# Kernel optimization log

Hardware: AMD Instinct MI355X
Metric: run time of the kernel (lower is better)

Reference implementation:

```python
import jax, jax.numpy as jnp
import numpy as np
from jax import lax

L, B, D = 2048, 16, 1024

def setup_inputs() -> dict:
    key = jax.random.key(0)
    k1, k2, k3 = jax.random.split(key, 3)
    prev_layer = jax.random.normal(k1, (L, B, D), dtype=jnp.float32)
    hidden = jax.random.normal(k2, (B, D), dtype=jnp.float32)
    W = jax.random.normal(k3, (3 * D, D), dtype=jnp.float32) * (1.0 / np.sqrt(D))
    b = jnp.zeros((3 * D,), dtype=jnp.float32)
    return {"prev_layer": prev_layer, "hidden": hidden, "W": W, "b": b}

def reference(prev_layer, hidden, W, b):
    # prev_layer: [L, B, D], hidden: [B, D], W: [3D, D], b: [3D]
    d = hidden.shape[-1]
    # nn.Linear: y = x @ W.T + b  (dropout p=0 -> identity)
    preact = jnp.einsum('lbi,oi->lbo', prev_layer, W) + b  # [L, B, 3D]
    x_t = preact[..., :d]                                   # candidate
    gates = jax.nn.sigmoid(preact[..., d:])                 # [L, B, 2D]
    z = gates[..., :d]
    h_gate = gates[..., d:]

    def step(h, zx):
        zt, xt = zx
        s = (1.0 - zt) * h + zt * xt
        return s, s

    hidden_final, ss = lax.scan(step, hidden, (z, x_t))     # ss: [L, B, D]
    out = (1.0 - h_gate) * ss + h_gate * prev_layer         # highway (input_size==output_size)
    return out, hidden_final
```

## Files before the change

### kernel.cpp

```cpp
#include <hip/hip_runtime.h>
#include <cstdint>

#define L_DIM 2048
#define B_DIM 16
#define D_DIM 1024
#define M_DIM (L_DIM*B_DIM)
#define N_DIM (3*D_DIM)
#define K_DIM D_DIM
#define NCH   (B_DIM*D_DIM)
#define SEG   64
#define SEGLEN (L_DIM/SEG)
#define CG    (NCH/8)

#define BK 64
#define NKT (K_DIM/BK)
#define BUF 65536

typedef __bf16 bf16x8 __attribute__((ext_vector_type(8)));
typedef float f32x4 __attribute__((ext_vector_type(4)));

__device__ inline float bf2f(ushort u){ return __uint_as_float(((unsigned)u)<<16); }
__device__ inline ushort f2bf(float f){
  unsigned u = __float_as_uint(f);
  u += 0x7fffu + ((u>>16)&1u);
  return (ushort)(u>>16);
}

__global__ __launch_bounds__(256) void cvt8(const float* __restrict__ in,
                                            ushort* __restrict__ out, int n8){
  int t = blockIdx.x*256 + threadIdx.x;
  if (t >= n8) return;
  const float4* p = (const float4*)(in + (size_t)t*8);
  float4 a = p[0], b = p[1];
  ushort r[8] = {f2bf(a.x),f2bf(a.y),f2bf(a.z),f2bf(a.w),
                 f2bf(b.x),f2bf(b.y),f2bf(b.z),f2bf(b.w)};
  *(uint4*)(out + (size_t)t*8) = *(const uint4*)r;
}

#define GLOAD(gp, lp) __builtin_amdgcn_global_load_lds( \
    (const __attribute__((address_space(1))) void*)(gp), \
    (__attribute__((address_space(3))) void*)(lp), 16, 0, 0)

__global__ __launch_bounds__(512, 2) void gemm_sru(
    const ushort* __restrict__ gA,
    const ushort* __restrict__ gB,
    const float* __restrict__ bias,
    ushort* __restrict__ xbuf, ushort* __restrict__ zbuf, ushort* __restrict__ hbuf)
{
  __shared__ ulong2 lds_[2*BUF/16];
  char* ldsb = (char*)lds_;

  const int tid  = threadIdx.x;
  const int lane = tid & 63, w = tid >> 6;
  const int wr = (w>>2)*64;
  const int wc = (w&3)*32;

  const int bid = blockIdx.x;
  const int swz = (bid & 7)*192 + (bid >> 3);
  const int bm = (swz / (N_DIM/256))*256, bn = (swz % (N_DIM/256))*256;

  const int l15 = lane & 15, l4 = lane >> 4, l7 = lane & 7;
  const int s0 = ((l4)     ^ l7) * 16;
  const int s1 = ((4 + l4) ^ l7) * 16;
  const char* pA0 = ldsb + (wr + l15)*128 + s0;
  const char* pA1 = ldsb + (wr + l15)*128 + s1;
  const char* pB0 = ldsb + 32768 + (wc + l15)*128 + s0;
  const char* pB1 = ldsb + 32768 + (wc + l15)*128 + s1;

  const int gks = (tid & 7) ^ ((tid >> 3) & 7);
  const size_t gArow = (size_t)(bm + (tid>>3))*K_DIM + gks*8;
  const size_t gBrow = (size_t)(bn + (tid>>3))*K_DIM + gks*8;

  f32x4 acc[4][8];
  #pragma unroll
  for (int i=0;i<4;i++)
    #pragma unroll
    for (int j=0;j<8;j++) acc[i][j] = (f32x4){0.f,0.f,0.f,0.f};

#define STAGE_A(h, tt) do{ \
    const ushort* g = gA + gArow + (size_t)(h)*128*K_DIM + (tt)*BK; \
    char* d = ldsb + ((tt)&1)*BUF + (h)*16384 + tid*16; \
    GLOAD(g, d); GLOAD(g + (size_t)64*K_DIM, d + 8192); \
  }while(0)
#define STAGE_B(h, tt) do{ \
    const ushort* g = gB + gBrow + (size_t)(h)*128*K_DIM + (tt)*BK; \
    char* d = ldsb + ((tt)&1)*BUF + 32768 + (h)*16384 + tid*16; \
    GLOAD(g, d); GLOAD(g + (size_t)64*K_DIM, d + 8192); \
  }while(0)

#define RD_A(dst, QA, bo) { _Pragma("unroll") \
    for (int fr=0; fr<4; ++fr){ \
      dst[fr][0] = *(const bf16x8*)(pA0 + (bo) + (QA)*16384 + fr*2048); \
      dst[fr][1] = *(const bf16x8*)(pA1 + (bo) + (QA)*16384 + fr*2048); } }
#define RD_B(QB, bo) { _Pragma("unroll") \
    for (int fc=0; fc<2; ++fc){ \
      b[fc][0] = *(const bf16x8*)(pB0 + (bo) + (QB)*16384 + fc*2048); \
      b[fc][1] = *(const bf16x8*)(pB1 + (bo) + (QB)*16384 + fc*2048); } }
#define MFMA_Q(qi, asrc) { \
    __builtin_amdgcn_s_setprio(1); \
    _Pragma("unroll") \
    for (int fr=0; fr<4; ++fr) \
      _Pragma("unroll") \
      for (int fc=0; fc<2; ++fc){ \
        acc[qi][fr*2+fc] = __builtin_amdgcn_mfma_f32_16x16x32_bf16(asrc[fr][0], b[fc][0], acc[qi][fr*2+fc], 0,0,0); \
        acc[qi][fr*2+fc] = __builtin_amdgcn_mfma_f32_16x16x32_bf16(asrc[fr][1], b[fc][1], acc[qi][fr*2+fc], 0,0,0); } \
    __builtin_amdgcn_s_setprio(0); }
#define BAR() asm volatile("" ::: "memory"); __builtin_amdgcn_s_barrier(); asm volatile("" ::: "memory")
#define VM(n) asm volatile("s_waitcnt vmcnt(" #n ")" ::: "memory")

  bf16x8 a0[4][2], a1[4][2], b[2][2];

  STAGE_A(0,0); STAGE_B(0,0); STAGE_A(1,0); STAGE_B(1,0);
  VM(4); BAR();

  for (int t = 0; t < NKT-1; ++t) {
    const int bo = (t&1)*BUF;
    RD_A(a0, 0, bo); RD_B(0, bo);
    STAGE_A(0, t+1);
    VM(4); BAR();
    MFMA_Q(0, a0); BAR();
    RD_A(a1, 1, bo);
    STAGE_B(0, t+1);
    VM(4); BAR();
    MFMA_Q(2, a1); BAR();
    RD_B(1, bo);
    STAGE_A(1, t+1);
    VM(6); BAR();
    MFMA_Q(3, a1); BAR();
    STAGE_B(1, t+1);
    VM(4); BAR();
    MFMA_Q(1, a0); BAR();
  }
  {
    const int bo = ((NKT-1)&1)*BUF;
    RD_A(a0, 0, bo); RD_B(0, bo);
    VM(2); BAR();
    MFMA_Q(0, a0); BAR();
    RD_A(a1, 1, bo);
    VM(0); BAR();
    MFMA_Q(2, a1); BAR();
    RD_B(1, bo);
    BAR();
    MFMA_Q(3, a1); BAR();
    MFMA_Q(1, a0); BAR();
  }

  const int region = bn >> 10;
  ushort* dst = region==0 ? xbuf : (region==1 ? zbuf : hbuf);
  ushort* lds16 = (ushort*)ldsb;
  float bv[2][2];
  #pragma unroll
  for (int qb=0; qb<2; ++qb)
    #pragma unroll
    for (int fc=0; fc<2; ++fc)
      bv[qb][fc] = bias[bn + qb*128 + wc + fc*16 + l15];

  #pragma unroll
  for (int qa=0; qa<2; ++qa)
    #pragma unroll
    for (int qb=0; qb<2; ++qb){
      const int qi = qa*2+qb;
      #pragma unroll
      for (int fr=0; fr<4; ++fr)
        #pragma unroll
        for (int fc=0; fc<2; ++fc)
          #pragma unroll
          for (int r=0; r<4; ++r){
            int row = qa*128 + wr + fr*16 + l4*4 + r;
            int col = qb*128 + wc + fc*16 + l15;
            float v = acc[qi][fr*2+fc][r] + bv[qb][fc];
            if (region) v = 1.f/(1.f + __expf(-v));
            lds16[row*256 + col] = f2bf(v);
          }
    }
  __syncthreads();
  const int cb = bn & (D_DIM-1);
  #pragma unroll
  for (int i=0;i<16;i++){
    int off = i*8192 + tid*16;
    int row = off >> 9;
    int cols = (off & 511) >> 1;
    *(uint4*)(dst + (size_t)(bm+row)*D_DIM + cb + cols) = *(const uint4*)(ldsb + off);
  }
#undef STAGE_A
#undef STAGE_B
#undef RD_A
#undef RD_B
#undef MFMA_Q
#undef BAR
#undef VM
}

__global__ __launch_bounds__(256) void scan_pass1(
    const ushort* __restrict__ z, const ushort* __restrict__ x,
    float* __restrict__ Aout, float* __restrict__ Bout)
{
  int t = blockIdx.x*256 + threadIdx.x;
  int cg = t & (CG-1), g = t >> 11;
  int c0 = cg*8;
  size_t base = (size_t)g*SEGLEN*NCH + c0;
  float A[8], Bc[8];
  #pragma unroll
  for (int j=0;j<8;j++){ A[j]=1.f; Bc[j]=0.f; }
  #pragma unroll 4
  for (int i=0;i<SEGLEN;i++){
    uint4 zv = *(const uint4*)(z + base + (size_t)i*NCH);
    uint4 xv = *(const uint4*)(x + base + (size_t)i*NCH);
    const ushort* zp = (const ushort*)&zv;
    const ushort* xp = (const ushort*)&xv;
    #pragma unroll
    for (int j=0;j<8;j++){
      float zf = bf2f(zp[j]);
      float a  = 1.f - zf;
      float bb = zf * bf2f(xp[j]);
      Bc[j] = a*Bc[j] + bb;
      A[j]  = a*A[j];
    }
  }
  float* Ao = Aout + (size_t)g*NCH + c0;
  float* Bo = Bout + (size_t)g*NCH + c0;
  *(float4*)Ao     = make_float4(A[0],A[1],A[2],A[3]);
  *(float4*)(Ao+4) = make_float4(A[4],A[5],A[6],A[7]);
  *(float4*)Bo     = make_float4(Bc[0],Bc[1],Bc[2],Bc[3]);
  *(float4*)(Bo+4) = make_float4(Bc[4],Bc[5],Bc[6],Bc[7]);
}

__global__ __launch_bounds__(256) void scan_pass2(
    const float* __restrict__ A, const float* __restrict__ B,
    const float* __restrict__ h0, float* __restrict__ seg, float* __restrict__ hfin)
{
  int c = blockIdx.x*256 + threadIdx.x;
  float s = h0[c];
  #pragma unroll 8
  for (int g=0; g<SEG; g++){
    seg[(size_t)g*NCH + c] = s;
    s = A[(size_t)g*NCH + c]*s + B[(size_t)g*NCH + c];
  }
  hfin[c] = s;
}

__global__ __launch_bounds__(256) void scan_pass3(
    const ushort* __restrict__ z, const ushort* __restrict__ x, const ushort* __restrict__ hg,
    const float* __restrict__ prev, const float* __restrict__ seg,
    float* __restrict__ out)
{
  int t = blockIdx.x*256 + threadIdx.x;
  int cg = t & (CG-1), g = t >> 11;
  int c0 = cg*8;
  float s[8];
  *(float4*)s     = *(const float4*)(seg + (size_t)g*NCH + c0);
  *(float4*)(s+4) = *(const float4*)(seg + (size_t)g*NCH + c0 + 4);
  size_t base = (size_t)g*SEGLEN*NCH + c0;
  #pragma unroll 2
  for (int i=0;i<SEGLEN;i++){
    size_t idx = base + (size_t)i*NCH;
    uint4 zv = *(const uint4*)(z+idx);
    uint4 xv = *(const uint4*)(x+idx);
    uint4 hv = *(const uint4*)(hg+idx);
    float4 p0 = *(const float4*)(prev+idx);
    float4 p1 = *(const float4*)(prev+idx+4);
    const ushort* zp=(const ushort*)&zv;
    const ushort* xp=(const ushort*)&xv;
    const ushort* hp=(const ushort*)&hv;
    float pv[8] = {p0.x,p0.y,p0.z,p0.w,p1.x,p1.y,p1.z,p1.w};
    float o[8];
    #pragma unroll
    for (int j=0;j<8;j++){
      float zf = bf2f(zp[j]);
      s[j] += zf*(bf2f(xp[j]) - s[j]);
      float hf = bf2f(hp[j]);
      o[j] = s[j] + hf*(pv[j] - s[j]);
    }
    *(float4*)(out+idx)   = make_float4(o[0],o[1],o[2],o[3]);
    *(float4*)(out+idx+4) = make_float4(o[4],o[5],o[6],o[7]);
  }
}

extern "C" void kernel_launch(void* const* d_in, const int* in_sizes, int n_in,
                              void* d_out, int out_size, void* d_ws, size_t ws_size,
                              hipStream_t stream) {
  const float* prev = (const float*)d_in[0];
  const float* h0   = (const float*)d_in[1];
  const float* W    = (const float*)d_in[2];
  const float* bias = (const float*)d_in[3];
  float* out  = (float*)d_out;
  float* hfin = out + (size_t)M_DIM*D_DIM;

  char* ws = (char*)d_ws;
  ushort* Ab = (ushort*)ws;
  ushort* Wb = (ushort*)(ws + (size_t)M_DIM*K_DIM*2);
  ushort* xb = (ushort*)(ws + (size_t)M_DIM*K_DIM*2 + (size_t)N_DIM*K_DIM*2);
  ushort* zb = xb + (size_t)M_DIM*D_DIM;
  ushort* hb = zb + (size_t)M_DIM*D_DIM;
  float* Abuf = (float*)ws;
  float* Bbuf = Abuf + (size_t)SEG*NCH;
  float* segb = Bbuf + (size_t)SEG*NCH;

  cvt8<<<(M_DIM*K_DIM/8 + 255)/256, 256, 0, stream>>>(prev, Ab, M_DIM*K_DIM/8);
  cvt8<<<(N_DIM*K_DIM/8 + 255)/256, 256, 0, stream>>>(W,    Wb, N_DIM*K_DIM/8);
  gemm_sru<<<(M_DIM/256)*(N_DIM/256), 512, 0, stream>>>(Ab, Wb, bias, xb, zb, hb);
  scan_pass1<<<(CG*SEG)/256, 256, 0, stream>>>(zb, xb, Abuf, Bbuf);
  scan_pass2<<<NCH/256, 256, 0, stream>>>(Abuf, Bbuf, h0, segb, hfin);
  scan_pass3<<<(CG*SEG)/256, 256, 0, stream>>>(zb, xb, hb, prev, segb, out);
}
```

Before: 382.0 us.

## Restructure GEMM K-loop to two barriers per tile and swizzle epilogue LDS

Reworks the GEMM main loop to hold both B fragments in registers (b0/b1), so each K-tile runs four MFMA quadrants with only two barriers instead of eight. Global prefetch stages are interleaved between MFMA groups, and the last iteration is folded into the loop with guards. The epilogue LDS staging also gets an XOR swizzle to reduce bank conflicts on the bf16 writes. The extra B fragment registers raise register pressure, and the tighter sync relies on the vmcnt waits remaining correct for LDS buffer reuse.

```diff
diff --git a/kernel.cpp b/kernel.cpp
--- a/kernel.cpp
+++ b/kernel.cpp
@@ -92,57 +92,44 @@
     for (int fr=0; fr<4; ++fr){ \
       dst[fr][0] = *(const bf16x8*)(pA0 + (bo) + (QA)*16384 + fr*2048); \
       dst[fr][1] = *(const bf16x8*)(pA1 + (bo) + (QA)*16384 + fr*2048); } }
-#define RD_B(QB, bo) { _Pragma("unroll") \
+#define RD_B(dst, QB, bo) { _Pragma("unroll") \
     for (int fc=0; fc<2; ++fc){ \
-      b[fc][0] = *(const bf16x8*)(pB0 + (bo) + (QB)*16384 + fc*2048); \
-      b[fc][1] = *(const bf16x8*)(pB1 + (bo) + (QB)*16384 + fc*2048); } }
-#define MFMA_Q(qi, asrc) { \
+      dst[fc][0] = *(const bf16x8*)(pB0 + (bo) + (QB)*16384 + fc*2048); \
+      dst[fc][1] = *(const bf16x8*)(pB1 + (bo) + (QB)*16384 + fc*2048); } }
+#define MFMA_Q(qi, asrc, bsrc) { \
     __builtin_amdgcn_s_setprio(1); \
     _Pragma("unroll") \
     for (int fr=0; fr<4; ++fr) \
       _Pragma("unroll") \
       for (int fc=0; fc<2; ++fc){ \
-        acc[qi][fr*2+fc] = __builtin_amdgcn_mfma_f32_16x16x32_bf16(asrc[fr][0], b[fc][0], acc[qi][fr*2+fc], 0,0,0); \
-        acc[qi][fr*2+fc] = __builtin_amdgcn_mfma_f32_16x16x32_bf16(asrc[fr][1], b[fc][1], acc[qi][fr*2+fc], 0,0,0); } \
+        acc[qi][fr*2+fc] = __builtin_amdgcn_mfma_f32_16x16x32_bf16(asrc[fr][0], bsrc[fc][0], acc[qi][fr*2+fc], 0,0,0); \
+        acc[qi][fr*2+fc] = __builtin_amdgcn_mfma_f32_16x16x32_bf16(asrc[fr][1], bsrc[fc][1], acc[qi][fr*2+fc], 0,0,0); } \
     __builtin_amdgcn_s_setprio(0); }
 #define BAR() asm volatile("" ::: "memory"); __builtin_amdgcn_s_barrier(); asm volatile("" ::: "memory")
 #define VM(n) asm volatile("s_waitcnt vmcnt(" #n ")" ::: "memory")
 
-  bf16x8 a0[4][2], a1[4][2], b[2][2];
+  bf16x8 a0[4][2], a1[4][2], b0[2][2], b1[2][2];
 
   STAGE_A(0,0); STAGE_B(0,0); STAGE_A(1,0); STAGE_B(1,0);
   VM(4); BAR();
 
-  for (int t = 0; t < NKT-1; ++t) {
+  for (int t = 0; t < NKT; ++t) {
     const int bo = (t&1)*BUF;
-    RD_A(a0, 0, bo); RD_B(0, bo);
-    STAGE_A(0, t+1);
-    VM(4); BAR();
-    MFMA_Q(0, a0); BAR();
+    RD_A(a0, 0, bo); RD_B(b0, 0, bo);
+    if (t < NKT-1) { STAGE_A(0, t+1); VM(2); }
+    else           { VM(0); }
+    BAR();
+    MFMA_Q(0, a0, b0);
+    RD_B(b1, 1, bo);
+    if (t < NKT-1) STAGE_B(0, t+1);
+    MFMA_Q(1, a0, b1);
     RD_A(a1, 1, bo);
-    STAGE_B(0, t+1);
-    VM(4); BAR();
-    MFMA_Q(2, a1); BAR();
-    RD_B(1, bo);
-    STAGE_A(1, t+1);
-    VM(6); BAR();
-    MFMA_Q(3, a1); BAR();
-    STAGE_B(1, t+1);
-    VM(4); BAR();
-    MFMA_Q(1, a0); BAR();
-  }
-  {
-    const int bo = ((NKT-1)&1)*BUF;
-    RD_A(a0, 0, bo); RD_B(0, bo);
-    VM(2); BAR();
-    MFMA_Q(0, a0); BAR();
-    RD_A(a1, 1, bo);
-    VM(0); BAR();
-    MFMA_Q(2, a1); BAR();
-    RD_B(1, bo);
+    if (t < NKT-1) STAGE_A(1, t+1);
+    MFMA_Q(2, a1, b0);
+    if (t < NKT-1) STAGE_B(1, t+1);
+    MFMA_Q(3, a1, b1);
+    if (t < NKT-1) VM(4);
     BAR();
-    MFMA_Q(3, a1); BAR();
-    MFMA_Q(1, a0); BAR();
   }
 
   const int region = bn >> 10;
@@ -170,7 +157,8 @@
             int col = qb*128 + wc + fc*16 + l15;
             float v = acc[qi][fr*2+fc][r] + bv[qb][fc];
             if (region) v = 1.f/(1.f + __expf(-v));
-            lds16[row*256 + col] = f2bf(v);
+            int slot = col >> 3;
+            lds16[row*256 + ((slot ^ (row&31))<<3) + (col&7)] = f2bf(v);
           }
     }
   __syncthreads();
@@ -179,8 +167,10 @@
   for (int i=0;i<16;i++){
     int off = i*8192 + tid*16;
     int row = off >> 9;
+    int slot = (off >> 4) & 31;
     int cols = (off & 511) >> 1;
-    *(uint4*)(dst + (size_t)(bm+row)*D_DIM + cb + cols) = *(const uint4*)(ldsb + off);
+    const char* src = ldsb + row*512 + ((slot ^ (row&31))<<4);
+    *(uint4*)(dst + (size_t)(bm+row)*D_DIM + cb + cols) = *(const uint4*)src;
   }
 #undef STAGE_A
 #undef STAGE_B
```

Result: no change. 386.7 us (+1.2%).
